# Kernel optimization log

Measured on AMD Instinct MI355X. Metric: run time of the kernel, lower is better.

The kernel has to match this reference:

```python
import jax, jax.numpy as jnp
import numpy as np

EMBED_DIM = 256
BATCH = 2
SEQ = 1024


def setup_inputs() -> dict:
    key = jax.random.key(0)
    ks = jax.random.split(key, 9)
    d = EMBED_DIM
    s = 1.0 / np.sqrt(d)
    return {
        "x": jax.random.normal(ks[0], (BATCH, SEQ, d), dtype=jnp.float32),
        "Wq": jax.random.uniform(ks[1], (d, d), jnp.float32, -s, s),
        "bq": jax.random.uniform(ks[2], (d,), jnp.float32, -s, s),
        "Wk": jax.random.uniform(ks[3], (d, d), jnp.float32, -s, s),
        "bk": jax.random.uniform(ks[4], (d,), jnp.float32, -s, s),
        "Wv": jax.random.uniform(ks[5], (d, d), jnp.float32, -s, s),
        "bv": jax.random.uniform(ks[6], (d,), jnp.float32, -s, s),
        "Wo": jax.random.uniform(ks[7], (d, d), jnp.float32, -s, s),
        "bo": jax.random.uniform(ks[8], (d,), jnp.float32, -s, s),
    }


def reference(x, Wq, bq, Wk, bk, Wv, bv, Wo, bo):
    d = x.shape[-1]
    Q = x @ Wq.T + bq  # (B,S,D)
    K = x @ Wk.T + bk
    V = x @ Wv.T + bv
    # geodesic_distance with metric='exponential': L2 norm of pairwise diffs
    diff = Q[:, :, None, :] - K[:, None, :, :]          # (B,S,S,D)
    dist = jnp.sqrt(jnp.sum(diff * diff, axis=-1))      # (B,S,S)
    attn = jax.nn.softmax(-dist / jnp.sqrt(jnp.float32(d)), axis=-1)
    attended = jnp.einsum('bqk,bkd->bqd', attn, V)      # (B,S,D)
    return attended @ Wo.T + bo
```

## Files before the change

### kernel.cpp

```cpp
#include <hip/hip_runtime.h>
#include <hip/hip_bf16.h>

#define BB 2
#define SS 1024
#define DD 256

typedef __attribute__((ext_vector_type(8))) short bf16x8;
typedef __attribute__((ext_vector_type(4))) float f32x4;

__device__ __forceinline__ unsigned short f2bf(float f) {
    __hip_bfloat16 h = __float2bfloat16(f);
    return *reinterpret_cast<unsigned short*>(&h);
}
__device__ __forceinline__ float bf2f(unsigned short u) {
    __hip_bfloat16 h;
    *reinterpret_cast<unsigned short*>(&h) = u;
    return __bfloat162float(h);
}
__device__ __forceinline__ bf16x8 cvt8(float4 f0, float4 f1) {
    bf16x8 o;
    o[0] = (short)f2bf(f0.x); o[1] = (short)f2bf(f0.y);
    o[2] = (short)f2bf(f0.z); o[3] = (short)f2bf(f0.w);
    o[4] = (short)f2bf(f1.x); o[5] = (short)f2bf(f1.y);
    o[6] = (short)f2bf(f1.z); o[7] = (short)f2bf(f1.w);
    return o;
}

__global__ __launch_bounds__(256) void cvt_bf16(
    const float* __restrict__ x,
    const float* __restrict__ Wq, const float* __restrict__ Wk,
    const float* __restrict__ Wv, const float* __restrict__ Wo,
    unsigned short* __restrict__ xb,
    unsigned short* __restrict__ Wqb, unsigned short* __restrict__ Wkb,
    unsigned short* __restrict__ Wvb, unsigned short* __restrict__ Wob)
{
    const int u = blockIdx.x * 256 + threadIdx.x;
    const float* src;
    unsigned short* dst;
    int base;
    if (u < 65536)      { src = x;  dst = xb;  base = u; }
    else if (u < 73728) { src = Wq; dst = Wqb; base = u - 65536; }
    else if (u < 81920) { src = Wk; dst = Wkb; base = u - 73728; }
    else if (u < 90112) { src = Wv; dst = Wvb; base = u - 81920; }
    else                { src = Wo; dst = Wob; base = u - 90112; }
    const float4* s4 = (const float4*)src + (size_t)base * 2;
    *(bf16x8*)(dst + (size_t)base * 8) = cvt8(s4[0], s4[1]);
}

__global__ __launch_bounds__(256, 2) void qkv_mfma(
    const unsigned short* __restrict__ xb,
    const unsigned short* __restrict__ Wqb, const float* __restrict__ bq,
    const unsigned short* __restrict__ Wkb, const float* __restrict__ bk,
    const unsigned short* __restrict__ Wvb, const float* __restrict__ bv,
    unsigned short* __restrict__ Qb, unsigned short* __restrict__ Kb,
    unsigned short* __restrict__ VB,
    float* __restrict__ qq, float* __restrict__ kk)
{
    __shared__ float red[4][16];
    const int t = threadIdx.x;
    const int w = t >> 6, l = t & 63, lr = l & 15, lc = l >> 4;
    const int bx = blockIdx.x;
    const int mat = bx % 3;
    const int rest = bx / 3;
    const int tile = rest >> 1;
    const int ch = rest & 1;
    const int r0 = tile * 16;
    const int b = r0 >> 10;
    const int s_in_base = r0 & (SS - 1);
    const size_t rows = (size_t)BB * SS;

    const unsigned short* W = (mat == 0) ? Wqb : (mat == 1) ? Wkb : Wvb;
    const float* bias       = (mat == 0) ? bq  : (mat == 1) ? bk  : bv;

    bf16x8 af[8];
#pragma unroll
    for (int db = 0; db < 8; ++db)
        af[db] = *(const bf16x8*)(xb + (size_t)(r0 + lr) * DD + db * 32 + 8 * lc);

    float nrm[4] = {0.f, 0.f, 0.f, 0.f};

#pragma unroll
    for (int cb = 0; cb < 2; ++cb) {
        const int jb = 128 * ch + 32 * w + 16 * cb;
        f32x4 acc = {0.f, 0.f, 0.f, 0.f};
#pragma unroll
        for (int db = 0; db < 8; ++db) {
            bf16x8 bf = *(const bf16x8*)(W + (size_t)(jb + lr) * DD + db * 32 + 8 * lc);
            acc = __builtin_amdgcn_mfma_f32_16x16x32_bf16(af[db], bf, acc, 0, 0, 0);
        }
        const float bv_ = bias[jb + lr];
#pragma unroll
        for (int r = 0; r < 4; ++r) {
            const int srow = r0 + lc * 4 + r;
            const float v = acc[r] + bv_;
            const unsigned short h = f2bf(v);
            if (mat == 0) {
                Qb[(size_t)srow * DD + jb + lr] = h;
                const float hv = bf2f(h); nrm[r] += hv * hv;
            } else if (mat == 1) {
                Kb[(size_t)srow * DD + jb + lr] = h;
                const float hv = bf2f(h); nrm[r] += hv * hv;
            } else {
                const int s_in = s_in_base + lc * 4 + r;
                const int kb32 = s_in >> 5;
                const int kslot = (s_in >> 3) & 3;
                const int jj = s_in & 7;
                const int db16 = ch * 8 + 2 * w + cb;
                const size_t off = ((size_t)((b * 32 + kb32) * 16 + db16) << 9)
                                 + ((kslot * 16 + lr) << 3) + jj;
                VB[off] = h;
            }
        }
    }

    if (mat < 2) {
#pragma unroll
        for (int r = 0; r < 4; ++r) {
            float n = nrm[r];
#pragma unroll
            for (int m = 1; m < 16; m <<= 1) n += __shfl_xor(n, m, 64);
            if (lr == 0) red[w][lc * 4 + r] = n;
        }
        __syncthreads();
        if (t < 16) {
            const float s = red[0][t] + red[1][t] + red[2][t] + red[3][t];
            if (mat == 0) qq[(size_t)ch * rows + r0 + t] = s;
            else          kk[(size_t)ch * rows + r0 + t] = s;
        }
    }
}

__global__ __launch_bounds__(512, 2) void attn_out_mfma(
    const unsigned short* __restrict__ Qb, const unsigned short* __restrict__ Kb,
    const unsigned short* __restrict__ VB,
    const float* __restrict__ qq, const float* __restrict__ kk,
    const unsigned short* __restrict__ Wob, const float* __restrict__ bo,
    float* __restrict__ out)
{
    __shared__ __align__(16) unsigned short P_s[16 * 1024];
    __shared__ float kk_s[SS];
    __shared__ float qq_s[16];
    __shared__ float es_red[8][16];
    __shared__ float inv_s[16];
    unsigned short* att_s = P_s;

    const int t = threadIdx.x;
    const int w = t >> 6, l = t & 63, lr = l & 15, lc = l >> 4;
    const int rowbase = blockIdx.x * 16;
    const int b = rowbase >> 10;
    const size_t rows = (size_t)BB * SS;

    kk_s[t]       = kk[b * SS + t]       + kk[rows + b * SS + t];
    kk_s[t + 512] = kk[b * SS + t + 512] + kk[rows + b * SS + t + 512];
    if (t < 16) qq_s[t] = qq[rowbase + t] + qq[rows + rowbase + t];

    bf16x8 qf[8];
#pragma unroll
    for (int db = 0; db < 8; ++db)
        qf[db] = *(const bf16x8*)(Qb + (size_t)(rowbase + lr) * DD + db * 32 + 8 * lc);

    __syncthreads();

    float psum[4] = {0.f, 0.f, 0.f, 0.f};
#pragma unroll
    for (int kbi = 0; kbi < 8; ++kbi) {
        const int kb = 128 * w + 16 * kbi;
        f32x4 acc = {0.f, 0.f, 0.f, 0.f};
#pragma unroll
        for (int db = 0; db < 8; ++db) {
            bf16x8 kf = *(const bf16x8*)(
                Kb + (size_t)(b * SS + kb + lr) * DD + db * 32 + 8 * lc);
            acc = __builtin_amdgcn_mfma_f32_16x16x32_bf16(qf[db], kf, acc, 0, 0, 0);
        }
        const int kcol = kb + lr;
        const float kkv = kk_s[kcol];
#pragma unroll
        for (int r = 0; r < 4; ++r) {
            const int qi = lc * 4 + r;
            const float d2 = fmaxf(qq_s[qi] + kkv - 2.f * acc[r], 0.f);
            const float e = __expf(-sqrtf(d2) * 0.0625f);
            psum[r] += e;
            P_s[qi * 1024 + (kcol ^ ((qi & 7) << 3))] = f2bf(e);
        }
    }
#pragma unroll
    for (int r = 0; r < 4; ++r) {
        float s = psum[r];
#pragma unroll
        for (int m = 1; m < 16; m <<= 1) s += __shfl_xor(s, m, 64);
        if (lr == 0) es_red[w][lc * 4 + r] = s;
    }
    __syncthreads();
    if (t < 16) {
        float s = 0.f;
#pragma unroll
        for (int ww = 0; ww < 8; ++ww) s += es_red[ww][t];
        inv_s[t] = 1.f / s;
    }

    f32x4 acc2[2];
#pragma unroll
    for (int i = 0; i < 2; ++i) acc2[i] = (f32x4){0.f, 0.f, 0.f, 0.f};

#pragma unroll
    for (int ki = 0; ki < 32; ++ki) {
        bf16x8 pf = *(const bf16x8*)(
            P_s + lr * 1024 + ((32 * ki + 8 * lc) ^ ((lr & 7) << 3)));
        const size_t tbase =
            ((size_t)((b * 32 + ki) * 16 + 2 * w) << 9) + l * 8;
#pragma unroll
        for (int dbi = 0; dbi < 2; ++dbi) {
            bf16x8 vf = *(const bf16x8*)(VB + tbase + ((size_t)dbi << 9));
            acc2[dbi] = __builtin_amdgcn_mfma_f32_16x16x32_bf16(pf, vf, acc2[dbi], 0, 0, 0);
        }
    }
    __syncthreads();

#pragma unroll
    for (int dbi = 0; dbi < 2; ++dbi)
#pragma unroll
        for (int r = 0; r < 4; ++r) {
            const int qi = lc * 4 + r;
            att_s[qi * 264 + 32 * w + 16 * dbi + lr] =
                f2bf(acc2[dbi][r] * inv_s[qi]);
        }
    __syncthreads();

    bf16x8 af[8];
#pragma unroll
    for (int db = 0; db < 8; ++db)
        af[db] = *(const bf16x8*)(att_s + lr * 264 + db * 32 + 8 * lc);

#pragma unroll
    for (int cb = 0; cb < 2; ++cb) {
        const int jb = 32 * w + 16 * cb;
        f32x4 acc = {0.f, 0.f, 0.f, 0.f};
#pragma unroll
        for (int db = 0; db < 8; ++db) {
            bf16x8 bf = *(const bf16x8*)(Wob + (size_t)(jb + lr) * DD + db * 32 + 8 * lc);
            acc = __builtin_amdgcn_mfma_f32_16x16x32_bf16(af[db], bf, acc, 0, 0, 0);
        }
        const float bov = bo[jb + lr];
#pragma unroll
        for (int r = 0; r < 4; ++r)
            out[(size_t)(rowbase + lc * 4 + r) * DD + jb + lr] = acc[r] + bov;
    }
}

extern "C" void kernel_launch(void* const* d_in, const int* in_sizes, int n_in,
                              void* d_out, int out_size, void* d_ws, size_t ws_size,
                              hipStream_t stream) {
    const float* x  = (const float*)d_in[0];
    const float* Wq = (const float*)d_in[1];
    const float* bq = (const float*)d_in[2];
    const float* Wk = (const float*)d_in[3];
    const float* bk = (const float*)d_in[4];
    const float* Wv = (const float*)d_in[5];
    const float* bv = (const float*)d_in[6];
    const float* Wo = (const float*)d_in[7];
    const float* bo = (const float*)d_in[8];
    float* out = (float*)d_out;

    const size_t rows = (size_t)BB * SS;
    unsigned short* Qb  = (unsigned short*)d_ws;
    unsigned short* Kb  = Qb + rows * DD;
    unsigned short* VB  = Kb + rows * DD;
    unsigned short* xb  = VB + rows * DD;
    unsigned short* Wqb = xb + rows * DD;
    unsigned short* Wkb = Wqb + (size_t)DD * DD;
    unsigned short* Wvb = Wkb + (size_t)DD * DD;
    unsigned short* Wob = Wvb + (size_t)DD * DD;
    float* qq    = (float*)(Wob + (size_t)DD * DD);
    float* kk    = qq + 2 * rows;

    cvt_bf16<<<384, 256, 0, stream>>>(x, Wq, Wk, Wv, Wo,
                                      xb, Wqb, Wkb, Wvb, Wob);
    qkv_mfma<<<768, 256, 0, stream>>>(
        xb, Wqb, bq, Wkb, bk, Wvb, bv, Qb, Kb, VB, qq, kk);
    attn_out_mfma<<<(int)(rows / 16), 512, 0, stream>>>(
        Qb, Kb, VB, qq, kk, Wob, bo, out);
}
```

Baseline: 50.65 us.

## Fuse Q projection into attention kernel and convert x to bf16 on load

The Q projection and its squared-norm reduction move into the attention kernel, which computes its 16-row Q tile from x and Wq into shared memory. The Q and qq global round trips disappear, and the projection kernel now produces only K and V. The separate x-to-bf16 conversion pass is removed; x is converted from fp32 as it is loaded, so the pre-pass converts only the weights. Each attention block now does extra MFMA work and an extra barrier before the QK loop, and reuses P_s as Q staging.

Measured after the change: 56.70 us. 11.9% more time.

```diff
diff --git a/kernel.cpp b/kernel.cpp
--- a/kernel.cpp
+++ b/kernel.cpp
@@ -26,11 +26,9 @@
     return o;
 }
 
-__global__ __launch_bounds__(256) void cvt_bf16(
-    const float* __restrict__ x,
+__global__ __launch_bounds__(256) void cvt_w(
     const float* __restrict__ Wq, const float* __restrict__ Wk,
     const float* __restrict__ Wv, const float* __restrict__ Wo,
-    unsigned short* __restrict__ xb,
     unsigned short* __restrict__ Wqb, unsigned short* __restrict__ Wkb,
     unsigned short* __restrict__ Wvb, unsigned short* __restrict__ Wob)
 {
@@ -38,30 +36,27 @@
     const float* src;
     unsigned short* dst;
     int base;
-    if (u < 65536)      { src = x;  dst = xb;  base = u; }
-    else if (u < 73728) { src = Wq; dst = Wqb; base = u - 65536; }
-    else if (u < 81920) { src = Wk; dst = Wkb; base = u - 73728; }
-    else if (u < 90112) { src = Wv; dst = Wvb; base = u - 81920; }
-    else                { src = Wo; dst = Wob; base = u - 90112; }
+    if (u < 8192)       { src = Wq; dst = Wqb; base = u; }
+    else if (u < 16384) { src = Wk; dst = Wkb; base = u - 8192; }
+    else if (u < 24576) { src = Wv; dst = Wvb; base = u - 16384; }
+    else                { src = Wo; dst = Wob; base = u - 24576; }
     const float4* s4 = (const float4*)src + (size_t)base * 2;
     *(bf16x8*)(dst + (size_t)base * 8) = cvt8(s4[0], s4[1]);
 }
 
-__global__ __launch_bounds__(256, 2) void qkv_mfma(
-    const unsigned short* __restrict__ xb,
-    const unsigned short* __restrict__ Wqb, const float* __restrict__ bq,
+__global__ __launch_bounds__(256, 2) void kv_mfma(
+    const float* __restrict__ x,
     const unsigned short* __restrict__ Wkb, const float* __restrict__ bk,
     const unsigned short* __restrict__ Wvb, const float* __restrict__ bv,
-    unsigned short* __restrict__ Qb, unsigned short* __restrict__ Kb,
-    unsigned short* __restrict__ VB,
-    float* __restrict__ qq, float* __restrict__ kk)
+    unsigned short* __restrict__ Kb, unsigned short* __restrict__ VB,
+    float* __restrict__ kk)
 {
     __shared__ float red[4][16];
     const int t = threadIdx.x;
     const int w = t >> 6, l = t & 63, lr = l & 15, lc = l >> 4;
     const int bx = blockIdx.x;
-    const int mat = bx % 3;
-    const int rest = bx / 3;
+    const int mat = bx & 1;
+    const int rest = bx >> 1;
     const int tile = rest >> 1;
     const int ch = rest & 1;
     const int r0 = tile * 16;
@@ -69,13 +64,15 @@
     const int s_in_base = r0 & (SS - 1);
     const size_t rows = (size_t)BB * SS;
 
-    const unsigned short* W = (mat == 0) ? Wqb : (mat == 1) ? Wkb : Wvb;
-    const float* bias       = (mat == 0) ? bq  : (mat == 1) ? bk  : bv;
+    const unsigned short* W = (mat == 0) ? Wkb : Wvb;
+    const float* bias       = (mat == 0) ? bk  : bv;
 
     bf16x8 af[8];
 #pragma unroll
-    for (int db = 0; db < 8; ++db)
-        af[db] = *(const bf16x8*)(xb + (size_t)(r0 + lr) * DD + db * 32 + 8 * lc);
+    for (int db = 0; db < 8; ++db) {
+        const float* xp = x + (size_t)(r0 + lr) * DD + db * 32 + 8 * lc;
+        af[db] = cvt8(*(const float4*)(xp), *(const float4*)(xp + 4));
+    }
 
     float nrm[4] = {0.f, 0.f, 0.f, 0.f};
 
@@ -95,9 +92,6 @@
             const float v = acc[r] + bv_;
             const unsigned short h = f2bf(v);
             if (mat == 0) {
-                Qb[(size_t)srow * DD + jb + lr] = h;
-                const float hv = bf2f(h); nrm[r] += hv * hv;
-            } else if (mat == 1) {
                 Kb[(size_t)srow * DD + jb + lr] = h;
                 const float hv = bf2f(h); nrm[r] += hv * hv;
             } else {
@@ -113,7 +107,7 @@
         }
     }
 
-    if (mat < 2) {
+    if (mat == 0) {
 #pragma unroll
         for (int r = 0; r < 4; ++r) {
             float n = nrm[r];
@@ -122,18 +116,17 @@
             if (lr == 0) red[w][lc * 4 + r] = n;
         }
         __syncthreads();
-        if (t < 16) {
-            const float s = red[0][t] + red[1][t] + red[2][t] + red[3][t];
-            if (mat == 0) qq[(size_t)ch * rows + r0 + t] = s;
-            else          kk[(size_t)ch * rows + r0 + t] = s;
-        }
+        if (t < 16)
+            kk[(size_t)ch * rows + r0 + t] =
+                red[0][t] + red[1][t] + red[2][t] + red[3][t];
     }
 }
 
 __global__ __launch_bounds__(512, 2) void attn_out_mfma(
-    const unsigned short* __restrict__ Qb, const unsigned short* __restrict__ Kb,
-    const unsigned short* __restrict__ VB,
-    const float* __restrict__ qq, const float* __restrict__ kk,
+    const float* __restrict__ x,
+    const unsigned short* __restrict__ Wqb, const float* __restrict__ bq,
+    const unsigned short* __restrict__ Kb, const unsigned short* __restrict__ VB,
+    const float* __restrict__ kk,
     const unsigned short* __restrict__ Wob, const float* __restrict__ bo,
     float* __restrict__ out)
 {
@@ -142,6 +135,7 @@
     __shared__ float qq_s[16];
     __shared__ float es_red[8][16];
     __shared__ float inv_s[16];
+    unsigned short* Q_s   = P_s;
     unsigned short* att_s = P_s;
 
     const int t = threadIdx.x;
@@ -152,13 +146,51 @@
 
     kk_s[t]       = kk[b * SS + t]       + kk[rows + b * SS + t];
     kk_s[t + 512] = kk[b * SS + t + 512] + kk[rows + b * SS + t + 512];
-    if (t < 16) qq_s[t] = qq[rowbase + t] + qq[rows + rowbase + t];
-
+
+    bf16x8 xf[8];
+#pragma unroll
+    for (int db = 0; db < 8; ++db) {
+        const float* xp = x + (size_t)(rowbase + lr) * DD + db * 32 + 8 * lc;
+        xf[db] = cvt8(*(const float4*)(xp), *(const float4*)(xp + 4));
+    }
+    float nrm[4] = {0.f, 0.f, 0.f, 0.f};
+#pragma unroll
+    for (int cb = 0; cb < 2; ++cb) {
+        const int jb = 32 * w + 16 * cb;
+        f32x4 acc = {0.f, 0.f, 0.f, 0.f};
+#pragma unroll
+        for (int db = 0; db < 8; ++db) {
+            bf16x8 bf = *(const bf16x8*)(Wqb + (size_t)(jb + lr) * DD + db * 32 + 8 * lc);
+            acc = __builtin_amdgcn_mfma_f32_16x16x32_bf16(xf[db], bf, acc, 0, 0, 0);
+        }
+        const float bqv = bq[jb + lr];
+#pragma unroll
+        for (int r = 0; r < 4; ++r) {
+            const int row = lc * 4 + r;
+            const float v = acc[r] + bqv;
+            const unsigned short h = f2bf(v);
+            Q_s[row * 264 + jb + lr] = h;
+            const float hv = bf2f(h); nrm[r] += hv * hv;
+        }
+    }
+#pragma unroll
+    for (int r = 0; r < 4; ++r) {
+        float n = nrm[r];
+#pragma unroll
+        for (int m = 1; m < 16; m <<= 1) n += __shfl_xor(n, m, 64);
+        if (lr == 0) es_red[w][lc * 4 + r] = n;
+    }
+    __syncthreads();
+    if (t < 16) {
+        float s = 0.f;
+#pragma unroll
+        for (int ww = 0; ww < 8; ++ww) s += es_red[ww][t];
+        qq_s[t] = s;
+    }
     bf16x8 qf[8];
 #pragma unroll
     for (int db = 0; db < 8; ++db)
-        qf[db] = *(const bf16x8*)(Qb + (size_t)(rowbase + lr) * DD + db * 32 + 8 * lc);
-
+        qf[db] = *(const bf16x8*)(Q_s + lr * 264 + db * 32 + 8 * lc);
     __syncthreads();
 
     float psum[4] = {0.f, 0.f, 0.f, 0.f};
@@ -262,21 +294,16 @@
     float* out = (float*)d_out;
 
     const size_t rows = (size_t)BB * SS;
-    unsigned short* Qb  = (unsigned short*)d_ws;
-    unsigned short* Kb  = Qb + rows * DD;
+    unsigned short* Kb  = (unsigned short*)d_ws;
     unsigned short* VB  = Kb + rows * DD;
-    unsigned short* xb  = VB + rows * DD;
-    unsigned short* Wqb = xb + rows * DD;
+    unsigned short* Wqb = VB + rows * DD;
     unsigned short* Wkb = Wqb + (size_t)DD * DD;
     unsigned short* Wvb = Wkb + (size_t)DD * DD;
     unsigned short* Wob = Wvb + (size_t)DD * DD;
-    float* qq    = (float*)(Wob + (size_t)DD * DD);
-    float* kk    = qq + 2 * rows;
-
-    cvt_bf16<<<384, 256, 0, stream>>>(x, Wq, Wk, Wv, Wo,
-                                      xb, Wqb, Wkb, Wvb, Wob);
-    qkv_mfma<<<768, 256, 0, stream>>>(
-        xb, Wqb, bq, Wkb, bk, Wvb, bv, Qb, Kb, VB, qq, kk);
+    float* kk    = (float*)(Wob + (size_t)DD * DD);
+
+    cvt_w<<<128, 256, 0, stream>>>(Wq, Wk, Wv, Wo, Wqb, Wkb, Wvb, Wob);
+    kv_mfma<<<512, 256, 0, stream>>>(x, Wkb, bk, Wvb, bv, Kb, VB, kk);
     attn_out_mfma<<<(int)(rows / 16), 512, 0, stream>>>(
-        Qb, Kb, VB, qq, kk, Wob, bo, out);
-}
+        x, Wqb, bq, Kb, VB, kk, Wob, bo, out);
+}
```
